# Optimization experiments

Measured on AMD Instinct MI355X. Metric: run time of the kernel, lower is better.

## Reference

```python
import jax, jax.numpy as jnp
import numpy as np

N_NODES = 100000
N_EDGES = 3200000
HID = 64


def setup_inputs() -> dict:
    key = jax.random.key(0)
    ks = jax.random.split(key, 20)
    x = jax.random.normal(ks[0], (N_NODES, 3), dtype=jnp.float32)
    edge_index = jax.random.randint(ks[1], (2, N_EDGES), 0, N_NODES, dtype=jnp.int32)

    def glorot(k, fan_in, fan_out):
        s = jnp.sqrt(6.0 / (fan_in + fan_out))
        return jax.random.uniform(k, (fan_in, fan_out), jnp.float32, -s, s)

    W_in = glorot(ks[2], 3, HID)
    b_in = jnp.zeros((HID,), jnp.float32)
    W_hid = jnp.stack([glorot(ks[3 + i], HID, HID) for i in range(6)])  # [6,64,64]
    b_hid = jnp.zeros((6, HID), jnp.float32)
    W_out = glorot(ks[10], HID, 6)
    b_out = jnp.zeros((6,), jnp.float32)
    return {"x": x, "edge_index": edge_index, "W_in": W_in, "b_in": b_in,
            "W_hid": W_hid, "b_hid": b_hid, "W_out": W_out, "b_out": b_out}


def _gcn_layer(x, W, b, src, dst, norm):
    # PyG GCNConv: h = x @ W; out[dst] += norm * h[src]; out += b
    h = x @ W
    msg = h[src] * norm[:, None]            # [E+N, F]
    agg = jax.ops.segment_sum(msg, dst, num_segments=N_NODES)
    return agg + b


def reference(x, edge_index, W_in, b_in, W_hid, b_hid, W_out, b_out):
    # Add self-loops and symmetric normalization (computed once, shared by all layers)
    loops = jnp.arange(N_NODES, dtype=edge_index.dtype)
    src = jnp.concatenate([edge_index[0], loops])
    dst = jnp.concatenate([edge_index[1], loops])
    deg = jax.ops.segment_sum(jnp.ones_like(dst, dtype=x.dtype), dst, num_segments=N_NODES)
    dinv = jnp.where(deg > 0, jax.lax.rsqrt(deg), 0.0)
    norm = dinv[src] * dinv[dst]            # [E+N]

    h = jax.nn.relu(_gcn_layer(x, W_in, b_in, src, dst, norm))
    for i in range(6):
        h = jax.nn.relu(_gcn_layer(h, W_hid[i], b_hid[i], src, dst, norm))
    # dropout p=0.25 with train=False -> identity (eval mode)
    out = _gcn_layer(h, W_out, b_out, src, dst, norm)
    return jax.nn.sigmoid(out)
```

## Files before the change

### kernel.cpp

```cpp
#include <hip/hip_runtime.h>
#include <hip/hip_fp16.h>
#include <math.h>

#define MAXBKT 512


__global__ __launch_bounds__(256) void k_bcount(const int* __restrict__ dstA,
                                                int E, int N, int nbkt, int* bucketCnt) {
    __shared__ int cnt[MAXBKT];
    for (int i = threadIdx.x; i < nbkt; i += 256) cnt[i] = 0;
    __syncthreads();
    int total = E + N;
    for (int i = blockIdx.x * 256 + threadIdx.x; i < total; i += gridDim.x * 256) {
        int d = (i < E) ? dstA[i] : (i - E);
        atomicAdd(&cnt[d >> 8], 1);
    }
    __syncthreads();
    for (int i = threadIdx.x; i < nbkt; i += 256)
        if (cnt[i]) atomicAdd(&bucketCnt[i], cnt[i]);
}

__global__ __launch_bounds__(MAXBKT) void k_bscan(const int* __restrict__ bucketCnt,
                                                  int* bucketOff, int* bucketCur,
                                                  int nbkt, int total) {
    __shared__ int sm[MAXBKT];
    int tid = threadIdx.x;
    int v = (tid < nbkt) ? bucketCnt[tid] : 0;
    sm[tid] = v;
    __syncthreads();
    for (int off = 1; off < MAXBKT; off <<= 1) {
        int t = 0;
        if (tid >= off) t = sm[tid - off];
        __syncthreads();
        sm[tid] += t;
        __syncthreads();
    }
    if (tid < nbkt) {
        int excl = sm[tid] - v;
        bucketOff[tid] = excl;
        bucketCur[tid] = excl;
    }
    if (tid == 0) bucketOff[nbkt] = total;
}

__global__ __launch_bounds__(256) void k_bscat2(const int* __restrict__ srcA,
                                                const int* __restrict__ dstA,
                                                int* bucketCur, unsigned int* bedges,
                                                int E, int N, int nbkt, int chunk) {
    __shared__ int cnt[MAXBKT];
    __shared__ int base[MAXBKT];
    int total = E + N;
    int lo = blockIdx.x * chunk;
    int hi = lo + chunk; if (hi > total) hi = total;
    for (int i = threadIdx.x; i < nbkt; i += 256) cnt[i] = 0;
    __syncthreads();
    for (int i = lo + threadIdx.x; i < hi; i += 256) {
        int d = (i < E) ? dstA[i] : (i - E);
        atomicAdd(&cnt[d >> 8], 1);
    }
    __syncthreads();
    for (int i = threadIdx.x; i < nbkt; i += 256) {
        base[i] = cnt[i] ? atomicAdd(&bucketCur[i], cnt[i]) : 0;
        cnt[i] = 0;
    }
    __syncthreads();
    for (int i = lo + threadIdx.x; i < hi; i += 256) {
        int s, d;
        if (i < E) { s = srcA[i]; d = dstA[i]; }
        else       { s = d = i - E; }
        int b = d >> 8;
        int pos = base[b] + atomicAdd(&cnt[b], 1);
        bedges[pos] = ((unsigned int)(d & 255) << 24) | (unsigned int)s;
    }
}

__global__ __launch_bounds__(256) void k_bfill2(const unsigned int* __restrict__ bedges,
                                                const int* __restrict__ bucketOff,
                                                int* __restrict__ rowptr,
                                                float* __restrict__ dinv,
                                                int* __restrict__ col,
                                                int N, int total) {
    __shared__ int ldeg[256];
    __shared__ int lcur[256];
    int b = blockIdx.x;
    int tid = threadIdx.x;
    int bo = bucketOff[b], be = bucketOff[b + 1];
    ldeg[tid] = 0;
    __syncthreads();
    for (int j = bo + tid; j < be; j += 256)
        atomicAdd(&ldeg[bedges[j] >> 24], 1);
    __syncthreads();
    int dg = ldeg[tid];
    lcur[tid] = dg;
    __syncthreads();
    for (int off = 1; off < 256; off <<= 1) {
        int t = 0;
        if (tid >= off) t = lcur[tid - off];
        __syncthreads();
        lcur[tid] += t;
        __syncthreads();
    }
    int excl = lcur[tid] - dg;
    int node = (b << 8) + tid;
    if (node < N) {
        rowptr[node] = bo + excl;
        dinv[node] = dg > 0 ? rsqrtf((float)dg) : 0.0f;
    }
    if (b == 0 && tid == 0) rowptr[N] = total;
    __syncthreads();
    lcur[tid] = bo + excl;
    __syncthreads();
    for (int j = bo + tid; j < be; j += 256) {
        unsigned int e = bedges[j];
        int pos = atomicAdd(&lcur[e >> 24], 1);
        col[pos] = (int)(e & 0x00FFFFFFu);
    }
}


__global__ __launch_bounds__(256) void k_xscale(const float* __restrict__ x,
                                                const float* __restrict__ dinv,
                                                float* __restrict__ xs, int n) {
    int i = blockIdx.x * 256 + threadIdx.x;
    if (i >= n) return;
    float dv = dinv[i];
    xs[i * 3 + 0] = dv * x[i * 3 + 0];
    xs[i * 3 + 1] = dv * x[i * 3 + 1];
    xs[i * 3 + 2] = dv * x[i * 3 + 2];
}

__global__ __launch_bounds__(256) void k_agg3(const float* __restrict__ xs,
                                              const int* __restrict__ rowptr,
                                              const int* __restrict__ col,
                                              const float* __restrict__ dinv,
                                              float* __restrict__ out3, int n) {
    int i = blockIdx.x * 256 + threadIdx.x;
    if (i >= n) return;
    float a0 = 0.f, a1 = 0.f, a2 = 0.f;
    int beg = rowptr[i], end = rowptr[i + 1];
    for (int j = beg; j < end; ++j) {
        int s = col[j];
        a0 += xs[s * 3 + 0];
        a1 += xs[s * 3 + 1];
        a2 += xs[s * 3 + 2];
    }
    float dv = dinv[i];
    out3[i * 3 + 0] = dv * a0;
    out3[i * 3 + 1] = dv * a1;
    out3[i * 3 + 2] = dv * a2;
}

__global__ __launch_bounds__(256) void k_tin(const float* __restrict__ agg3v,
                                             const float* __restrict__ Win,
                                             const float* __restrict__ bin,
                                             __half* __restrict__ h, int n) {
    int idx = blockIdx.x * 256 + threadIdx.x;
    int node = idx >> 6, f = idx & 63;
    if (node >= n) return;
    float v = bin[f];
    v += agg3v[node * 3 + 0] * Win[0 * 64 + f];
    v += agg3v[node * 3 + 1] * Win[1 * 64 + f];
    v += agg3v[node * 3 + 2] * Win[2 * 64 + f];
    h[(size_t)node * 64 + f] = __float2half(fmaxf(v, 0.f));
}

__global__ __launch_bounds__(256) void k_matmul64(const __half* __restrict__ h,
                                                  const float* __restrict__ W,
                                                  const float* __restrict__ dinv,
                                                  __half* __restrict__ t16, int n) {
    __shared__ float Wl[64 * 64];
    __shared__ float Hl[16][68];
    int tid = threadIdx.x;
    for (int i = tid * 4; i < 4096; i += 1024)
        *(float4*)&Wl[i] = *(const float4*)&W[i];
    int nodeBase = blockIdx.x * 16;
    {
        int idx = tid * 4;
        int nl = idx >> 6, k = idx & 63;
        int node = nodeBase + nl;
        float4 v = make_float4(0.f, 0.f, 0.f, 0.f);
        if (node < n) {
            float2 raw = *(const float2*)&h[(size_t)node * 64 + k];
            const __half2* hp = (const __half2*)&raw;
            float2 p0 = __half22float2(hp[0]);
            float2 p1 = __half22float2(hp[1]);
            v = make_float4(p0.x, p0.y, p1.x, p1.y);
        }
        *(float4*)&Hl[nl][k] = v;
    }
    __syncthreads();
    int nl = tid >> 4;
    int fq = (tid & 15) * 4;
    float4 acc = make_float4(0.f, 0.f, 0.f, 0.f);
#pragma unroll
    for (int k = 0; k < 64; ++k) {
        float hv = Hl[nl][k];
        float4 wv = *(const float4*)&Wl[k * 64 + fq];
        acc.x += hv * wv.x;
        acc.y += hv * wv.y;
        acc.z += hv * wv.z;
        acc.w += hv * wv.w;
    }
    int node = nodeBase + nl;
    if (node < n) {
        float dv = dinv[node];
        __half2* dst = (__half2*)&t16[(size_t)node * 64 + fq];
        dst[0] = __floats2half2_rn(acc.x * dv, acc.y * dv);
        dst[1] = __floats2half2_rn(acc.z * dv, acc.w * dv);
    }
}

__global__ __launch_bounds__(256) void k_agg64(const __half* __restrict__ t16,
                                               const int* __restrict__ rowptr,
                                               const int* __restrict__ col,
                                               const float* __restrict__ dinv,
                                               const float* __restrict__ bias,
                                               __half* __restrict__ hout, int n) {
    int node = blockIdx.x * 4 + ((int)threadIdx.x >> 6);
    if (node >= n) return;
    int lane = threadIdx.x & 63;
    int slot = lane >> 3;
    int fl   = lane & 7;
    int beg = rowptr[node], end = rowptr[node + 1];
    float a0 = 0.f, a1 = 0.f, a2 = 0.f, a3 = 0.f, a4 = 0.f, a5 = 0.f, a6 = 0.f, a7 = 0.f;
    int j = beg + slot;
    for (; j + 8 < end; j += 16) {
        int s0 = col[j];
        int s1 = col[j + 8];
        float4 r0 = *(const float4*)(t16 + (size_t)s0 * 64 + fl * 8);
        float4 r1 = *(const float4*)(t16 + (size_t)s1 * 64 + fl * 8);
        const __half2* h0 = (const __half2*)&r0;
        const __half2* h1 = (const __half2*)&r1;
        float2 p;
        p = __half22float2(h0[0]); a0 += p.x; a1 += p.y;
        p = __half22float2(h0[1]); a2 += p.x; a3 += p.y;
        p = __half22float2(h0[2]); a4 += p.x; a5 += p.y;
        p = __half22float2(h0[3]); a6 += p.x; a7 += p.y;
        p = __half22float2(h1[0]); a0 += p.x; a1 += p.y;
        p = __half22float2(h1[1]); a2 += p.x; a3 += p.y;
        p = __half22float2(h1[2]); a4 += p.x; a5 += p.y;
        p = __half22float2(h1[3]); a6 += p.x; a7 += p.y;
    }
    if (j < end) {
        int s0 = col[j];
        float4 r0 = *(const float4*)(t16 + (size_t)s0 * 64 + fl * 8);
        const __half2* h0 = (const __half2*)&r0;
        float2 p;
        p = __half22float2(h0[0]); a0 += p.x; a1 += p.y;
        p = __half22float2(h0[1]); a2 += p.x; a3 += p.y;
        p = __half22float2(h0[2]); a4 += p.x; a5 += p.y;
        p = __half22float2(h0[3]); a6 += p.x; a7 += p.y;
    }
#pragma unroll
    for (int m = 8; m < 64; m <<= 1) {
        a0 += __shfl_xor(a0, m, 64);
        a1 += __shfl_xor(a1, m, 64);
        a2 += __shfl_xor(a2, m, 64);
        a3 += __shfl_xor(a3, m, 64);
        a4 += __shfl_xor(a4, m, 64);
        a5 += __shfl_xor(a5, m, 64);
        a6 += __shfl_xor(a6, m, 64);
        a7 += __shfl_xor(a7, m, 64);
    }
    if (slot == 0) {
        float dv = dinv[node];
        int fo = fl * 8;
        __half2 w0 = __floats2half2_rn(fmaxf(dv * a0 + bias[fo + 0], 0.f),
                                       fmaxf(dv * a1 + bias[fo + 1], 0.f));
        __half2 w1 = __floats2half2_rn(fmaxf(dv * a2 + bias[fo + 2], 0.f),
                                       fmaxf(dv * a3 + bias[fo + 3], 0.f));
        __half2 w2 = __floats2half2_rn(fmaxf(dv * a4 + bias[fo + 4], 0.f),
                                       fmaxf(dv * a5 + bias[fo + 5], 0.f));
        __half2 w3 = __floats2half2_rn(fmaxf(dv * a6 + bias[fo + 6], 0.f),
                                       fmaxf(dv * a7 + bias[fo + 7], 0.f));
        __half2* dst = (__half2*)&hout[(size_t)node * 64 + fo];
        dst[0] = w0; dst[1] = w1; dst[2] = w2; dst[3] = w3;
    }
}

__global__ __launch_bounds__(256) void k_tout(const __half* __restrict__ h,
                                              const float* __restrict__ Wout,
                                              const float* __restrict__ dinv,
                                              __half* __restrict__ t6p, int n) {
    __shared__ float Wl6[64 * 6];
    for (int i = threadIdx.x; i < 384; i += 256) Wl6[i] = Wout[i];
    __syncthreads();
    int node = blockIdx.x * 256 + threadIdx.x;
    if (node >= n) return;
    float acc[6] = {0.f, 0.f, 0.f, 0.f, 0.f, 0.f};
#pragma unroll
    for (int k4 = 0; k4 < 16; ++k4) {
        float2 raw = *(const float2*)&h[(size_t)node * 64 + k4 * 4];
        const __half2* hp = (const __half2*)&raw;
        float2 p0 = __half22float2(hp[0]);
        float2 p1 = __half22float2(hp[1]);
        float hq[4] = {p0.x, p0.y, p1.x, p1.y};
#pragma unroll
        for (int q = 0; q < 4; ++q) {
            int k = k4 * 4 + q;
#pragma unroll
            for (int f = 0; f < 6; ++f) acc[f] += hq[q] * Wl6[k * 6 + f];
        }
    }
    float dv = dinv[node];
    __half2 o0 = __floats2half2_rn(dv * acc[0], dv * acc[1]);
    __half2 o1 = __floats2half2_rn(dv * acc[2], dv * acc[3]);
    __half2 o2 = __floats2half2_rn(dv * acc[4], dv * acc[5]);
    __half2 o3 = __floats2half2_rn(0.f, 0.f);
    __half2* dst = (__half2*)&t6p[(size_t)node * 8];
    dst[0] = o0; dst[1] = o1; dst[2] = o2; dst[3] = o3;
}

__global__ __launch_bounds__(256) void k_agg6(const __half* __restrict__ t6p,
                                              const int* __restrict__ rowptr,
                                              const int* __restrict__ col,
                                              const float* __restrict__ dinv,
                                              const float* __restrict__ bout,
                                              float* __restrict__ out, int n) {
    int i = blockIdx.x * 256 + threadIdx.x;
    if (i >= n) return;
    float a0 = 0.f, a1 = 0.f, a2 = 0.f, a3 = 0.f, a4 = 0.f, a5 = 0.f;
    int beg = rowptr[i], end = rowptr[i + 1];
    int j = beg;
    for (; j + 1 < end; j += 2) {
        int s0 = col[j], s1 = col[j + 1];
        float4 r0 = *(const float4*)(t6p + (size_t)s0 * 8);
        float4 r1 = *(const float4*)(t6p + (size_t)s1 * 8);
        const __half2* h0 = (const __half2*)&r0;
        const __half2* h1 = (const __half2*)&r1;
        float2 p;
        p = __half22float2(h0[0]); a0 += p.x; a1 += p.y;
        p = __half22float2(h0[1]); a2 += p.x; a3 += p.y;
        p = __half22float2(h0[2]); a4 += p.x; a5 += p.y;
        p = __half22float2(h1[0]); a0 += p.x; a1 += p.y;
        p = __half22float2(h1[1]); a2 += p.x; a3 += p.y;
        p = __half22float2(h1[2]); a4 += p.x; a5 += p.y;
    }
    if (j < end) {
        int s0 = col[j];
        float4 r0 = *(const float4*)(t6p + (size_t)s0 * 8);
        const __half2* h0 = (const __half2*)&r0;
        float2 p;
        p = __half22float2(h0[0]); a0 += p.x; a1 += p.y;
        p = __half22float2(h0[1]); a2 += p.x; a3 += p.y;
        p = __half22float2(h0[2]); a4 += p.x; a5 += p.y;
    }
    float dv = dinv[i];
    out[i * 6 + 0] = 1.0f / (1.0f + expf(-(dv * a0 + bout[0])));
    out[i * 6 + 1] = 1.0f / (1.0f + expf(-(dv * a1 + bout[1])));
    out[i * 6 + 2] = 1.0f / (1.0f + expf(-(dv * a2 + bout[2])));
    out[i * 6 + 3] = 1.0f / (1.0f + expf(-(dv * a3 + bout[3])));
    out[i * 6 + 4] = 1.0f / (1.0f + expf(-(dv * a4 + bout[4])));
    out[i * 6 + 5] = 1.0f / (1.0f + expf(-(dv * a5 + bout[5])));
}


extern "C" void kernel_launch(void* const* d_in, const int* in_sizes, int n_in,
                              void* d_out, int out_size, void* d_ws, size_t ws_size,
                              hipStream_t stream) {
    const float* x    = (const float*)d_in[0];
    const int*   eidx = (const int*)d_in[1];
    const float* Win  = (const float*)d_in[2];
    const float* bin  = (const float*)d_in[3];
    const float* Whid = (const float*)d_in[4];
    const float* bhid = (const float*)d_in[5];
    const float* Wout = (const float*)d_in[6];
    const float* bout = (const float*)d_in[7];
    float* out = (float*)d_out;

    const int N = in_sizes[0] / 3;
    const int E = in_sizes[1] / 2;
    const int* srcA = eidx;
    const int* dstA = eidx + E;
    const int TOT = E + N;
    const int NBKT = (N + 255) >> 8;

    char* p = (char*)d_ws;
    auto alloc = [&](size_t bytes) -> void* {
        void* r = (void*)p;
        p += (bytes + 255) & ~(size_t)255;
        return r;
    };
    float*        dinv      = (float*)alloc((size_t)N * 4);
    int*          rowptr    = (int*)alloc((size_t)(N + 1) * 4);
    int*          bucketCnt = (int*)alloc((size_t)MAXBKT * 4);
    int*          bucketOff = (int*)alloc((size_t)(MAXBKT + 1) * 4);
    int*          bucketCur = (int*)alloc((size_t)MAXBKT * 4);
    unsigned int* bedges    = (unsigned int*)alloc((size_t)TOT * 4);
    int*          col       = (int*)alloc((size_t)TOT * 4);
    float*        xs        = (float*)alloc((size_t)N * 3 * 4);
    float*        agg3buf   = (float*)alloc((size_t)N * 3 * 4);
    __half*       hbuf      = (__half*)alloc((size_t)N * 64 * 2);
    __half*       t16       = (__half*)alloc((size_t)N * 64 * 2);
    __half*       t6p       = (__half*)alloc((size_t)N * 8 * 2);

    const int NB_N = (N + 255) / 256;

    hipMemsetAsync(bucketCnt, 0, (size_t)MAXBKT * 4, stream);
    k_bcount<<<256, 256, 0, stream>>>(dstA, E, N, NBKT, bucketCnt);
    k_bscan<<<1, MAXBKT, 0, stream>>>(bucketCnt, bucketOff, bucketCur, NBKT, TOT);
    const int CHUNK = (TOT + 255) / 256;
    k_bscat2<<<256, 256, 0, stream>>>(srcA, dstA, bucketCur, bedges, E, N, NBKT, CHUNK);
    k_bfill2<<<NBKT, 256, 0, stream>>>(bedges, bucketOff, rowptr, dinv, col, N, TOT);

    k_xscale<<<NB_N, 256, 0, stream>>>(x, dinv, xs, N);
    k_agg3<<<NB_N, 256, 0, stream>>>(xs, rowptr, col, dinv, agg3buf, N);
    k_tin<<<(N * 64 + 255) / 256, 256, 0, stream>>>(agg3buf, Win, bin, hbuf, N);

    for (int i = 0; i < 6; ++i) {
        k_matmul64<<<(N + 15) / 16, 256, 0, stream>>>(hbuf, Whid + (size_t)i * 4096, dinv, t16, N);
        k_agg64<<<(N + 3) / 4, 256, 0, stream>>>(t16, rowptr, col, dinv, bhid + (size_t)i * 64, hbuf, N);
    }

    k_tout<<<NB_N, 256, 0, stream>>>(hbuf, Wout, dinv, t6p, N);
    k_agg6<<<NB_N, 256, 0, stream>>>(t6p, rowptr, col, dinv, bout, out, N);
}
```

Baseline: 726.1 us.

## Fuse aggregation with next layer's matmul and fold xscale into CSR fill

Each hidden-layer aggregation now applies bias and ReLU into shared memory and immediately multiplies by the next layer's weight matrix, so the intermediate fp16 hidden buffer is never written or reread. The input transform, the last aggregation with the output projection, and the x pre-scaling with the CSR fill are fused the same way, which removes several launches. The bucket count and scatter kernels also move from 256 to 512 blocks. In exchange, each 16-node block loads a 16 KB weight tile and each wave handles four nodes one after another, which may lower parallelism inside the latency-bound gather.

```diff
diff --git a/kernel.cpp b/kernel.cpp
--- a/kernel.cpp
+++ b/kernel.cpp
@@ -76,8 +76,10 @@
 
 __global__ __launch_bounds__(256) void k_bfill2(const unsigned int* __restrict__ bedges,
                                                 const int* __restrict__ bucketOff,
+                                                const float* __restrict__ x,
                                                 int* __restrict__ rowptr,
                                                 float* __restrict__ dinv,
+                                                float* __restrict__ xs,
                                                 int* __restrict__ col,
                                                 int N, int total) {
     __shared__ int ldeg[256];
@@ -104,7 +106,11 @@
     int node = (b << 8) + tid;
     if (node < N) {
         rowptr[node] = bo + excl;
-        dinv[node] = dg > 0 ? rsqrtf((float)dg) : 0.0f;
+        float dv = dg > 0 ? rsqrtf((float)dg) : 0.0f;
+        dinv[node] = dv;
+        xs[node * 3 + 0] = dv * x[node * 3 + 0];
+        xs[node * 3 + 1] = dv * x[node * 3 + 1];
+        xs[node * 3 + 2] = dv * x[node * 3 + 2];
     }
     if (b == 0 && tid == 0) rowptr[N] = total;
     __syncthreads();
@@ -117,17 +123,6 @@
     }
 }
 
-
-__global__ __launch_bounds__(256) void k_xscale(const float* __restrict__ x,
-                                                const float* __restrict__ dinv,
-                                                float* __restrict__ xs, int n) {
-    int i = blockIdx.x * 256 + threadIdx.x;
-    if (i >= n) return;
-    float dv = dinv[i];
-    xs[i * 3 + 0] = dv * x[i * 3 + 0];
-    xs[i * 3 + 1] = dv * x[i * 3 + 1];
-    xs[i * 3 + 2] = dv * x[i * 3 + 2];
-}
 
 __global__ __launch_bounds__(256) void k_agg3(const float* __restrict__ xs,
                                               const int* __restrict__ rowptr,
@@ -150,43 +145,37 @@
     out3[i * 3 + 2] = dv * a2;
 }
 
-__global__ __launch_bounds__(256) void k_tin(const float* __restrict__ agg3v,
-                                             const float* __restrict__ Win,
-                                             const float* __restrict__ bin,
-                                             __half* __restrict__ h, int n) {
-    int idx = blockIdx.x * 256 + threadIdx.x;
-    int node = idx >> 6, f = idx & 63;
-    if (node >= n) return;
-    float v = bin[f];
-    v += agg3v[node * 3 + 0] * Win[0 * 64 + f];
-    v += agg3v[node * 3 + 1] * Win[1 * 64 + f];
-    v += agg3v[node * 3 + 2] * Win[2 * 64 + f];
-    h[(size_t)node * 64 + f] = __float2half(fmaxf(v, 0.f));
-}
-
-__global__ __launch_bounds__(256) void k_matmul64(const __half* __restrict__ h,
-                                                  const float* __restrict__ W,
-                                                  const float* __restrict__ dinv,
-                                                  __half* __restrict__ t16, int n) {
+__global__ __launch_bounds__(256) void k_tin_mm(const float* __restrict__ agg3v,
+                                                const float* __restrict__ Win,
+                                                const float* __restrict__ bin,
+                                                const float* __restrict__ W0,
+                                                const float* __restrict__ dinv,
+                                                __half* __restrict__ tout, int n) {
     __shared__ float Wl[64 * 64];
     __shared__ float Hl[16][68];
     int tid = threadIdx.x;
     for (int i = tid * 4; i < 4096; i += 1024)
-        *(float4*)&Wl[i] = *(const float4*)&W[i];
+        *(float4*)&Wl[i] = *(const float4*)&W0[i];
     int nodeBase = blockIdx.x * 16;
     {
         int idx = tid * 4;
-        int nl = idx >> 6, k = idx & 63;
+        int nl = idx >> 6, f0 = idx & 63;
         int node = nodeBase + nl;
-        float4 v = make_float4(0.f, 0.f, 0.f, 0.f);
+        float a0 = 0.f, a1 = 0.f, a2 = 0.f;
         if (node < n) {
-            float2 raw = *(const float2*)&h[(size_t)node * 64 + k];
-            const __half2* hp = (const __half2*)&raw;
-            float2 p0 = __half22float2(hp[0]);
-            float2 p1 = __half22float2(hp[1]);
-            v = make_float4(p0.x, p0.y, p1.x, p1.y);
-        }
-        *(float4*)&Hl[nl][k] = v;
+            a0 = agg3v[node * 3 + 0];
+            a1 = agg3v[node * 3 + 1];
+            a2 = agg3v[node * 3 + 2];
+        }
+        float4 hv;
+        float* hp = (float*)&hv;
+#pragma unroll
+        for (int q = 0; q < 4; ++q) {
+            int f = f0 + q;
+            float v = bin[f] + a0 * Win[f] + a1 * Win[64 + f] + a2 * Win[128 + f];
+            hp[q] = fmaxf(v, 0.f);
+        }
+        *(float4*)&Hl[nl][f0] = hv;
     }
     __syncthreads();
     int nl = tid >> 4;
@@ -204,111 +193,207 @@
     int node = nodeBase + nl;
     if (node < n) {
         float dv = dinv[node];
-        __half2* dst = (__half2*)&t16[(size_t)node * 64 + fq];
+        __half2* dst = (__half2*)&tout[(size_t)node * 64 + fq];
         dst[0] = __floats2half2_rn(acc.x * dv, acc.y * dv);
         dst[1] = __floats2half2_rn(acc.z * dv, acc.w * dv);
     }
 }
 
-__global__ __launch_bounds__(256) void k_agg64(const __half* __restrict__ t16,
-                                               const int* __restrict__ rowptr,
-                                               const int* __restrict__ col,
-                                               const float* __restrict__ dinv,
-                                               const float* __restrict__ bias,
-                                               __half* __restrict__ hout, int n) {
-    int node = blockIdx.x * 4 + ((int)threadIdx.x >> 6);
-    if (node >= n) return;
-    int lane = threadIdx.x & 63;
+__global__ __launch_bounds__(256) void k_aggmm64(const __half* __restrict__ tin,
+                                                 const int* __restrict__ rowptr,
+                                                 const int* __restrict__ col,
+                                                 const float* __restrict__ dinv,
+                                                 const float* __restrict__ bias,
+                                                 const float* __restrict__ W,
+                                                 __half* __restrict__ tnext, int n) {
+    __shared__ float Wl[64 * 64];
+    __shared__ float Hl[16][68];
+    int tid = threadIdx.x;
+    for (int i = tid * 4; i < 4096; i += 1024)
+        *(float4*)&Wl[i] = *(const float4*)&W[i];
+    int nodeBase = blockIdx.x * 16;
+    int wv = tid >> 6;
+    int lane = tid & 63;
     int slot = lane >> 3;
-    int fl   = lane & 7;
-    int beg = rowptr[node], end = rowptr[node + 1];
-    float a0 = 0.f, a1 = 0.f, a2 = 0.f, a3 = 0.f, a4 = 0.f, a5 = 0.f, a6 = 0.f, a7 = 0.f;
-    int j = beg + slot;
-    for (; j + 8 < end; j += 16) {
-        int s0 = col[j];
-        int s1 = col[j + 8];
-        float4 r0 = *(const float4*)(t16 + (size_t)s0 * 64 + fl * 8);
-        float4 r1 = *(const float4*)(t16 + (size_t)s1 * 64 + fl * 8);
-        const __half2* h0 = (const __half2*)&r0;
-        const __half2* h1 = (const __half2*)&r1;
-        float2 p;
-        p = __half22float2(h0[0]); a0 += p.x; a1 += p.y;
-        p = __half22float2(h0[1]); a2 += p.x; a3 += p.y;
-        p = __half22float2(h0[2]); a4 += p.x; a5 += p.y;
-        p = __half22float2(h0[3]); a6 += p.x; a7 += p.y;
-        p = __half22float2(h1[0]); a0 += p.x; a1 += p.y;
-        p = __half22float2(h1[1]); a2 += p.x; a3 += p.y;
-        p = __half22float2(h1[2]); a4 += p.x; a5 += p.y;
-        p = __half22float2(h1[3]); a6 += p.x; a7 += p.y;
-    }
-    if (j < end) {
-        int s0 = col[j];
-        float4 r0 = *(const float4*)(t16 + (size_t)s0 * 64 + fl * 8);
-        const __half2* h0 = (const __half2*)&r0;
-        float2 p;
-        p = __half22float2(h0[0]); a0 += p.x; a1 += p.y;
-        p = __half22float2(h0[1]); a2 += p.x; a3 += p.y;
-        p = __half22float2(h0[2]); a4 += p.x; a5 += p.y;
-        p = __half22float2(h0[3]); a6 += p.x; a7 += p.y;
-    }
-#pragma unroll
-    for (int m = 8; m < 64; m <<= 1) {
-        a0 += __shfl_xor(a0, m, 64);
-        a1 += __shfl_xor(a1, m, 64);
-        a2 += __shfl_xor(a2, m, 64);
-        a3 += __shfl_xor(a3, m, 64);
-        a4 += __shfl_xor(a4, m, 64);
-        a5 += __shfl_xor(a5, m, 64);
-        a6 += __shfl_xor(a6, m, 64);
-        a7 += __shfl_xor(a7, m, 64);
-    }
-    if (slot == 0) {
+    int fl = lane & 7;
+#pragma unroll
+    for (int k4 = 0; k4 < 4; ++k4) {
+        int nl = wv * 4 + k4;
+        int node = nodeBase + nl;
+        float a0 = 0.f, a1 = 0.f, a2 = 0.f, a3 = 0.f, a4 = 0.f, a5 = 0.f, a6 = 0.f, a7 = 0.f;
+        if (node < n) {
+            int beg = rowptr[node], end = rowptr[node + 1];
+            int j = beg + slot;
+            for (; j + 8 < end; j += 16) {
+                int s0 = col[j];
+                int s1 = col[j + 8];
+                float4 r0 = *(const float4*)(tin + (size_t)s0 * 64 + fl * 8);
+                float4 r1 = *(const float4*)(tin + (size_t)s1 * 64 + fl * 8);
+                const __half2* h0 = (const __half2*)&r0;
+                const __half2* h1 = (const __half2*)&r1;
+                float2 p;
+                p = __half22float2(h0[0]); a0 += p.x; a1 += p.y;
+                p = __half22float2(h0[1]); a2 += p.x; a3 += p.y;
+                p = __half22float2(h0[2]); a4 += p.x; a5 += p.y;
+                p = __half22float2(h0[3]); a6 += p.x; a7 += p.y;
+                p = __half22float2(h1[0]); a0 += p.x; a1 += p.y;
+                p = __half22float2(h1[1]); a2 += p.x; a3 += p.y;
+                p = __half22float2(h1[2]); a4 += p.x; a5 += p.y;
+                p = __half22float2(h1[3]); a6 += p.x; a7 += p.y;
+            }
+            if (j < end) {
+                int s0 = col[j];
+                float4 r0 = *(const float4*)(tin + (size_t)s0 * 64 + fl * 8);
+                const __half2* h0 = (const __half2*)&r0;
+                float2 p;
+                p = __half22float2(h0[0]); a0 += p.x; a1 += p.y;
+                p = __half22float2(h0[1]); a2 += p.x; a3 += p.y;
+                p = __half22float2(h0[2]); a4 += p.x; a5 += p.y;
+                p = __half22float2(h0[3]); a6 += p.x; a7 += p.y;
+            }
+        }
+#pragma unroll
+        for (int m = 8; m < 64; m <<= 1) {
+            a0 += __shfl_xor(a0, m, 64);
+            a1 += __shfl_xor(a1, m, 64);
+            a2 += __shfl_xor(a2, m, 64);
+            a3 += __shfl_xor(a3, m, 64);
+            a4 += __shfl_xor(a4, m, 64);
+            a5 += __shfl_xor(a5, m, 64);
+            a6 += __shfl_xor(a6, m, 64);
+            a7 += __shfl_xor(a7, m, 64);
+        }
+        if (slot == 0) {
+            float dv = (node < n) ? dinv[node] : 0.f;
+            int fo = fl * 8;
+            float4 w0, w1;
+            w0.x = fmaxf(dv * a0 + bias[fo + 0], 0.f);
+            w0.y = fmaxf(dv * a1 + bias[fo + 1], 0.f);
+            w0.z = fmaxf(dv * a2 + bias[fo + 2], 0.f);
+            w0.w = fmaxf(dv * a3 + bias[fo + 3], 0.f);
+            w1.x = fmaxf(dv * a4 + bias[fo + 4], 0.f);
+            w1.y = fmaxf(dv * a5 + bias[fo + 5], 0.f);
+            w1.z = fmaxf(dv * a6 + bias[fo + 6], 0.f);
+            w1.w = fmaxf(dv * a7 + bias[fo + 7], 0.f);
+            *(float4*)&Hl[nl][fo] = w0;
+            *(float4*)&Hl[nl][fo + 4] = w1;
+        }
+    }
+    __syncthreads();
+    int nl = tid >> 4;
+    int fq = (tid & 15) * 4;
+    float4 acc = make_float4(0.f, 0.f, 0.f, 0.f);
+#pragma unroll
+    for (int k = 0; k < 64; ++k) {
+        float hv = Hl[nl][k];
+        float4 wv = *(const float4*)&Wl[k * 64 + fq];
+        acc.x += hv * wv.x;
+        acc.y += hv * wv.y;
+        acc.z += hv * wv.z;
+        acc.w += hv * wv.w;
+    }
+    int node = nodeBase + nl;
+    if (node < n) {
         float dv = dinv[node];
-        int fo = fl * 8;
-        __half2 w0 = __floats2half2_rn(fmaxf(dv * a0 + bias[fo + 0], 0.f),
-                                       fmaxf(dv * a1 + bias[fo + 1], 0.f));
-        __half2 w1 = __floats2half2_rn(fmaxf(dv * a2 + bias[fo + 2], 0.f),
-                                       fmaxf(dv * a3 + bias[fo + 3], 0.f));
-        __half2 w2 = __floats2half2_rn(fmaxf(dv * a4 + bias[fo + 4], 0.f),
-                                       fmaxf(dv * a5 + bias[fo + 5], 0.f));
-        __half2 w3 = __floats2half2_rn(fmaxf(dv * a6 + bias[fo + 6], 0.f),
-                                       fmaxf(dv * a7 + bias[fo + 7], 0.f));
-        __half2* dst = (__half2*)&hout[(size_t)node * 64 + fo];
-        dst[0] = w0; dst[1] = w1; dst[2] = w2; dst[3] = w3;
-    }
-}
-
-__global__ __launch_bounds__(256) void k_tout(const __half* __restrict__ h,
-                                              const float* __restrict__ Wout,
-                                              const float* __restrict__ dinv,
-                                              __half* __restrict__ t6p, int n) {
+        __half2* dst = (__half2*)&tnext[(size_t)node * 64 + fq];
+        dst[0] = __floats2half2_rn(acc.x * dv, acc.y * dv);
+        dst[1] = __floats2half2_rn(acc.z * dv, acc.w * dv);
+    }
+}
+
+__global__ __launch_bounds__(256) void k_aggtout(const __half* __restrict__ tin,
+                                                 const int* __restrict__ rowptr,
+                                                 const int* __restrict__ col,
+                                                 const float* __restrict__ dinv,
+                                                 const float* __restrict__ bias,
+                                                 const float* __restrict__ Wout,
+                                                 __half* __restrict__ t6p, int n) {
     __shared__ float Wl6[64 * 6];
-    for (int i = threadIdx.x; i < 384; i += 256) Wl6[i] = Wout[i];
-    __syncthreads();
-    int node = blockIdx.x * 256 + threadIdx.x;
-    if (node >= n) return;
-    float acc[6] = {0.f, 0.f, 0.f, 0.f, 0.f, 0.f};
-#pragma unroll
-    for (int k4 = 0; k4 < 16; ++k4) {
-        float2 raw = *(const float2*)&h[(size_t)node * 64 + k4 * 4];
-        const __half2* hp = (const __half2*)&raw;
-        float2 p0 = __half22float2(hp[0]);
-        float2 p1 = __half22float2(hp[1]);
-        float hq[4] = {p0.x, p0.y, p1.x, p1.y};
-#pragma unroll
-        for (int q = 0; q < 4; ++q) {
-            int k = k4 * 4 + q;
-#pragma unroll
-            for (int f = 0; f < 6; ++f) acc[f] += hq[q] * Wl6[k * 6 + f];
-        }
-    }
-    float dv = dinv[node];
-    __half2 o0 = __floats2half2_rn(dv * acc[0], dv * acc[1]);
-    __half2 o1 = __floats2half2_rn(dv * acc[2], dv * acc[3]);
-    __half2 o2 = __floats2half2_rn(dv * acc[4], dv * acc[5]);
-    __half2 o3 = __floats2half2_rn(0.f, 0.f);
-    __half2* dst = (__half2*)&t6p[(size_t)node * 8];
-    dst[0] = o0; dst[1] = o1; dst[2] = o2; dst[3] = o3;
+    __shared__ float Hl[16][68];
+    int tid = threadIdx.x;
+    for (int i = tid; i < 384; i += 256) Wl6[i] = Wout[i];
+    int nodeBase = blockIdx.x * 16;
+    int wv = tid >> 6;
+    int lane = tid & 63;
+    int slot = lane >> 3;
+    int fl = lane & 7;
+#pragma unroll
+    for (int k4 = 0; k4 < 4; ++k4) {
+        int nl = wv * 4 + k4;
+        int node = nodeBase + nl;
+        float a0 = 0.f, a1 = 0.f, a2 = 0.f, a3 = 0.f, a4 = 0.f, a5 = 0.f, a6 = 0.f, a7 = 0.f;
+        if (node < n) {
+            int beg = rowptr[node], end = rowptr[node + 1];
+            int j = beg + slot;
+            for (; j + 8 < end; j += 16) {
+                int s0 = col[j];
+                int s1 = col[j + 8];
+                float4 r0 = *(const float4*)(tin + (size_t)s0 * 64 + fl * 8);
+                float4 r1 = *(const float4*)(tin + (size_t)s1 * 64 + fl * 8);
+                const __half2* h0 = (const __half2*)&r0;
+                const __half2* h1 = (const __half2*)&r1;
+                float2 p;
+                p = __half22float2(h0[0]); a0 += p.x; a1 += p.y;
+                p = __half22float2(h0[1]); a2 += p.x; a3 += p.y;
+                p = __half22float2(h0[2]); a4 += p.x; a5 += p.y;
+                p = __half22float2(h0[3]); a6 += p.x; a7 += p.y;
+                p = __half22float2(h1[0]); a0 += p.x; a1 += p.y;
+                p = __half22float2(h1[1]); a2 += p.x; a3 += p.y;
+                p = __half22float2(h1[2]); a4 += p.x; a5 += p.y;
+                p = __half22float2(h1[3]); a6 += p.x; a7 += p.y;
+            }
+            if (j < end) {
+                int s0 = col[j];
+                float4 r0 = *(const float4*)(tin + (size_t)s0 * 64 + fl * 8);
+                const __half2* h0 = (const __half2*)&r0;
+                float2 p;
+                p = __half22float2(h0[0]); a0 += p.x; a1 += p.y;
+                p = __half22float2(h0[1]); a2 += p.x; a3 += p.y;
+                p = __half22float2(h0[2]); a4 += p.x; a5 += p.y;
+                p = __half22float2(h0[3]); a6 += p.x; a7 += p.y;
+            }
+        }
+#pragma unroll
+        for (int m = 8; m < 64; m <<= 1) {
+            a0 += __shfl_xor(a0, m, 64);
+            a1 += __shfl_xor(a1, m, 64);
+            a2 += __shfl_xor(a2, m, 64);
+            a3 += __shfl_xor(a3, m, 64);
+            a4 += __shfl_xor(a4, m, 64);
+            a5 += __shfl_xor(a5, m, 64);
+            a6 += __shfl_xor(a6, m, 64);
+            a7 += __shfl_xor(a7, m, 64);
+        }
+        if (slot == 0) {
+            float dv = (node < n) ? dinv[node] : 0.f;
+            int fo = fl * 8;
+            float4 w0, w1;
+            w0.x = fmaxf(dv * a0 + bias[fo + 0], 0.f);
+            w0.y = fmaxf(dv * a1 + bias[fo + 1], 0.f);
+            w0.z = fmaxf(dv * a2 + bias[fo + 2], 0.f);
+            w0.w = fmaxf(dv * a3 + bias[fo + 3], 0.f);
+            w1.x = fmaxf(dv * a4 + bias[fo + 4], 0.f);
+            w1.y = fmaxf(dv * a5 + bias[fo + 5], 0.f);
+            w1.z = fmaxf(dv * a6 + bias[fo + 6], 0.f);
+            w1.w = fmaxf(dv * a7 + bias[fo + 7], 0.f);
+            *(float4*)&Hl[nl][fo] = w0;
+            *(float4*)&Hl[nl][fo + 4] = w1;
+        }
+    }
+    __syncthreads();
+    int nl = tid >> 4;
+    int f = tid & 15;
+    int node = nodeBase + nl;
+    if (node < n && f < 8) {
+        __half o = __float2half(0.f);
+        if (f < 6) {
+            float acc = 0.f;
+#pragma unroll
+            for (int k = 0; k < 64; ++k) acc += Hl[nl][k] * Wl6[k * 6 + f];
+            o = __float2half(dinv[node] * acc);
+        }
+        t6p[(size_t)node * 8 + f] = o;
+    }
 }
 
 __global__ __launch_bounds__(256) void k_agg6(const __half* __restrict__ t6p,
@@ -390,28 +475,34 @@
     int*          col       = (int*)alloc((size_t)TOT * 4);
     float*        xs        = (float*)alloc((size_t)N * 3 * 4);
     float*        agg3buf   = (float*)alloc((size_t)N * 3 * 4);
-    __half*       hbuf      = (__half*)alloc((size_t)N * 64 * 2);
-    __half*       t16       = (__half*)alloc((size_t)N * 64 * 2);
+    __half*       tA        = (__half*)alloc((size_t)N * 64 * 2);
+    __half*       tB        = (__half*)alloc((size_t)N * 64 * 2);
     __half*       t6p       = (__half*)alloc((size_t)N * 8 * 2);
 
     const int NB_N = (N + 255) / 256;
+    const int NB16 = (N + 15) / 16;
 
     hipMemsetAsync(bucketCnt, 0, (size_t)MAXBKT * 4, stream);
-    k_bcount<<<256, 256, 0, stream>>>(dstA, E, N, NBKT, bucketCnt);
+    k_bcount<<<512, 256, 0, stream>>>(dstA, E, N, NBKT, bucketCnt);
     k_bscan<<<1, MAXBKT, 0, stream>>>(bucketCnt, bucketOff, bucketCur, NBKT, TOT);
-    const int CHUNK = (TOT + 255) / 256;
-    k_bscat2<<<256, 256, 0, stream>>>(srcA, dstA, bucketCur, bedges, E, N, NBKT, CHUNK);
-    k_bfill2<<<NBKT, 256, 0, stream>>>(bedges, bucketOff, rowptr, dinv, col, N, TOT);
-
-    k_xscale<<<NB_N, 256, 0, stream>>>(x, dinv, xs, N);
+    const int CHUNK = (TOT + 511) / 512;
+    k_bscat2<<<512, 256, 0, stream>>>(srcA, dstA, bucketCur, bedges, E, N, NBKT, CHUNK);
+    k_bfill2<<<NBKT, 256, 0, stream>>>(bedges, bucketOff, x, rowptr, dinv, xs, col, N, TOT);
+
     k_agg3<<<NB_N, 256, 0, stream>>>(xs, rowptr, col, dinv, agg3buf, N);
-    k_tin<<<(N * 64 + 255) / 256, 256, 0, stream>>>(agg3buf, Win, bin, hbuf, N);
-
-    for (int i = 0; i < 6; ++i) {
-        k_matmul64<<<(N + 15) / 16, 256, 0, stream>>>(hbuf, Whid + (size_t)i * 4096, dinv, t16, N);
-        k_agg64<<<(N + 3) / 4, 256, 0, stream>>>(t16, rowptr, col, dinv, bhid + (size_t)i * 64, hbuf, N);
-    }
-
-    k_tout<<<NB_N, 256, 0, stream>>>(hbuf, Wout, dinv, t6p, N);
+    k_tin_mm<<<NB16, 256, 0, stream>>>(agg3buf, Win, bin, Whid, dinv, tA, N);
+
+    __half* tin = tA;
+    __half* tnx = tB;
+    for (int i = 1; i <= 5; ++i) {
+        k_aggmm64<<<NB16, 256, 0, stream>>>(tin, rowptr, col, dinv,
+                                            bhid + (size_t)(i - 1) * 64,
+                                            Whid + (size_t)i * 4096, tnx, N);
+        __half* tmp = tin; tin = tnx; tnx = tmp;
+    }
+
+    k_aggtout<<<NB16, 256, 0, stream>>>(tin, rowptr, col, dinv,
+                                        bhid + (size_t)5 * 64, Wout, t6p, N);
+
     k_agg6<<<NB_N, 256, 0, stream>>>(t6p, rowptr, col, dinv, bout, out, N);
 }
```

Result: faster. 683.3 us (-5.9%).
